# Performance work log

Measured on AMD Instinct MI355X. Metric: run time of the kernel, lower is better.

## Reference

```python
import jax, jax.numpy as jnp
import numpy as np

# Hardware-emulation constants (from init_kwargs, NeuroSim-style QLinear)
WL_IN = 8        # input activation bit width (bit-serial)
WL_W = 8         # weight bit width
CELL_BIT = 2     # bits per memory cell -> 4 weight slices
SUB = 128        # crossbar sub-array size (rows summed in analog)
ADC_BITS = 5     # ADC precision per partial sum
ONOFF = 10.0     # cell on/off conductance ratio
VARI = 0.05      # multiplicative device variation sigma


def _adc_quant(x, bits, axes):
    # LinearQuantizeOut: uniform quantization between tensor min/max
    mn = jnp.min(x, axis=axes, keepdims=True)
    mx = jnp.max(x, axis=axes, keepdims=True)
    step = (mx - mn) * (2.0 ** (-bits))
    step = jnp.where(step <= 0, 1.0, step)
    idx = jnp.clip(jnp.floor((x - mn) / step), 0.0, 2.0 ** bits - 1.0)
    return idx * step + mn


def _qlinear_hw(x, w, noise):
    """Analog PIM crossbar emulation of y = x @ w.T with bit-serial inputs,
    bit-sliced cells, on/off-ratio offset + dummy column, device variation,
    per-subarray ADC quantization."""
    B, N = x.shape
    F = w.shape[0]
    I, W, K = WL_IN, WL_W, WL_W // CELL_BIT
    cr = 2.0 ** CELL_BIT
    lower, upper = 1.0 / ONOFF, 1.0
    S = (N + SUB - 1) // SUB
    Np = S * SUB
    # quantize input to I bits in [0,1]; weight to W-bit integer in [0, 2^W-1]
    xq = jnp.round(jnp.clip(x, 0.0, 1.0) * (2.0 ** I - 1.0))            # [B, N]
    Xi = jnp.clip(jnp.round((w + 1.0) * 0.5 * (2.0 ** W - 1.0)), 0.0, 2.0 ** W - 1.0)  # [F, N]
    xq = jnp.pad(xq, ((0, 0), (0, Np - N)))
    Xi = jnp.pad(Xi, ((0, 0), (0, Np - N)))
    zpow = 2.0 ** jnp.arange(I, dtype=x.dtype)
    kpow = cr ** jnp.arange(K, dtype=x.dtype)
    bits = jnp.mod(jnp.floor(xq[..., None] / zpow), 2.0)                # [B, Np, I]
    slc = jnp.mod(jnp.floor(Xi[..., None] / kpow), cr)                  # [F, Np, K]
    g = slc * (upper - lower) + (cr - 1.0) * lower                      # cell conductances
    g = g * (1.0 + VARI * noise)                                        # device variation
    bits = bits.reshape(B, S, SUB, I)
    g = g.reshape(F, S, SUB, K)
    # analog partial sums per (input bit i, subarray s, weight slice k)
    P = jnp.einsum('bsai,fsak->iskbf', bits, g)                         # [I,S,K,B,F]
    # dummy column (all cells at lowest conductance), identical across F
    D = jnp.transpose(bits.sum(axis=2), (2, 1, 0)) * ((cr - 1.0) * lower)  # [I,S,B]
    Pq = _adc_quant(P, ADC_BITS, axes=(3, 4))
    Dq = _adc_quant(D, ADC_BITS, axes=(2,))
    scal = (2.0 ** jnp.arange(I, dtype=x.dtype))[:, None] * (cr ** jnp.arange(K, dtype=x.dtype))[None, :]
    acc = jnp.einsum('iskbf,ik->bf', Pq - Dq[:, :, None, :, None], scal) / (upper - lower)
    # undo integer mappings: w = 2*Xi/(2^W-1) - 1, x = xq/(2^I-1)
    out = 2.0 * acc / ((2.0 ** I - 1.0) * (2.0 ** W - 1.0)) \
          - xq.sum(axis=1, keepdims=True) / (2.0 ** I - 1.0)
    return out


def _qlinear(x, w, noise):
    # straight-through quantized weight (WAGE-style STE) + hardware forward
    Xi = jnp.clip(jnp.round((w + 1.0) * 0.5 * (2.0 ** WL_W - 1.0)), 0.0, 2.0 ** WL_W - 1.0)
    wq = 2.0 * Xi / (2.0 ** WL_W - 1.0) - 1.0
    wq_ste = w + jax.lax.stop_gradient(wq - w)
    out_ideal = x @ wq_ste.T
    out_hw = _qlinear_hw(x, w, noise)
    return out_ideal + jax.lax.stop_gradient(out_hw - out_ideal)


def setup_inputs() -> dict:
    key = jax.random.key(0)
    k1, k2, k3, k4, k5 = jax.random.split(key, 5)
    x = jax.random.uniform(k1, (1024, 784), dtype=jnp.float32)
    w1 = jax.random.normal(k2, (512, 784), dtype=jnp.float32) * 0.05
    w3 = jax.random.normal(k3, (10, 512), dtype=jnp.float32) * 0.08
    noise1 = jax.random.normal(k4, (512, 896, 4), dtype=jnp.float32)  # 784 padded to 7*128
    noise3 = jax.random.normal(k5, (10, 512, 4), dtype=jnp.float32)   # 512 = 4*128 exact
    return {"x": x, "w1": w1, "w3": w3, "noise1": noise1, "noise3": noise3}


def reference(x, w1, w3, noise1, noise3):
    h = jnp.tanh(_qlinear(x, w1, noise1))   # QLinear(784,512) + Tanh
    return _qlinear(h, w3, noise3)          # QLinear(512,10)
```

## Files before the change

kernel.cpp:

```cpp
#include <hip/hip_runtime.h>

#define FLTMAX 3.402823466e+38f


__global__ void init_kernel(float* __restrict__ acc1, unsigned* __restrict__ stats1)
{
    int gid = blockIdx.x * 256 + threadIdx.x;
    if (gid < 1024 * 512) acc1[gid] = 0.f;
    if (gid < 224) { stats1[gid * 2] = 0x7F7FFFFFu; stats1[gid * 2 + 1] = 0u; }
}

__global__ void prep1_kernel(const float* __restrict__ x, float* __restrict__ xq1,
                             float* __restrict__ sx1)
{
    __shared__ float red[128];
    int b = blockIdx.x;
    float psum = 0.f;
    for (int n = threadIdx.x; n < 896; n += 128) {
        float v = 0.f;
        if (n < 784) {
            float xv = x[b * 784 + n];
            xv = fminf(fmaxf(xv, 0.f), 1.f);
            v = rintf(__fmul_rn(xv, 255.f));
        }
        xq1[b * 896 + n] = v;
        psum += v;
    }
    red[threadIdx.x] = psum;
    __syncthreads();
    for (int w = 64; w >= 1; w >>= 1) {
        if (threadIdx.x < w) red[threadIdx.x] += red[threadIdx.x + w];
        __syncthreads();
    }
    if (threadIdx.x == 0) sx1[b] = red[0];
}

__global__ void bitpack_kernel(const float* __restrict__ xq1, unsigned* __restrict__ xqb)
{
    int gid = blockIdx.x * 256 + threadIdx.x;
    if (gid >= 1024 * 28) return;
    int b = gid / 28, w = gid % 28;
    unsigned words[8] = {0, 0, 0, 0, 0, 0, 0, 0};
    const float* src = &xq1[b * 896 + w * 32];
#pragma unroll 8
    for (int n = 0; n < 32; ++n) {
        int v = (int)src[n];
#pragma unroll
        for (int i = 0; i < 8; ++i) words[i] |= ((unsigned)((v >> i) & 1)) << n;
    }
#pragma unroll
    for (int i = 0; i < 8; ++i) xqb[(i * 1024 + b) * 28 + w] = words[i];
}

__global__ void prepg1t_kernel(const float* __restrict__ w1, const float* __restrict__ noise1,
                               float* __restrict__ g1t)
{
    __shared__ float t[4][32][33];
    const int n0 = blockIdx.x * 32, f0 = blockIdx.y * 32;
    const int tid = threadIdx.x;
    {
        int n = tid & 31, fi = tid >> 5;
#pragma unroll
        for (int p = 0; p < 4; ++p) {
            int f = p * 8 + fi;
            int gn = n0 + n, gf = f0 + f;
            float gv[4] = {0.f, 0.f, 0.f, 0.f};
            if (gn < 784) {
                float w = w1[gf * 784 + gn];
                float Xi = fminf(fmaxf(rintf(__fmul_rn(__fmul_rn(__fadd_rn(w, 1.f), 0.5f), 255.f)),
                                       0.f), 255.f);
                int xi = (int)Xi;
                float4 nz = *(const float4*)&noise1[(gf * 896 + gn) * 4];
                float nzv[4] = {nz.x, nz.y, nz.z, nz.w};
#pragma unroll
                for (int k = 0; k < 4; ++k) {
                    int slc = (xi >> (2 * k)) & 3;
                    float base = __fadd_rn(__fmul_rn((float)slc, 0.9f), 0.3f);
                    float nf = __fadd_rn(1.f, __fmul_rn(0.05f, nzv[k]));
                    gv[k] = __fmul_rn(base, nf);
                }
            }
#pragma unroll
            for (int k = 0; k < 4; ++k) t[k][n][f] = gv[k];
        }
    }
    __syncthreads();
    {
        int f = tid & 31, nn = tid >> 5;
#pragma unroll
        for (int p = 0; p < 4; ++p) {
            int n = p * 8 + nn;
#pragma unroll
            for (int k = 0; k < 4; ++k)
                g1t[(n0 + n) * 2048 + k * 512 + f0 + f] = t[k][n][f];
        }
    }
}

__global__ void prepg2_kernel(const float* __restrict__ w3, const float* __restrict__ noise3,
                              float* __restrict__ g2t)
{
    int gid = blockIdx.x * 256 + threadIdx.x;
    if (gid >= 10 * 512) return;
    int f = gid / 512, n = gid % 512;
    float w = w3[f * 512 + n];
    float Xi = fminf(fmaxf(rintf(__fmul_rn(__fmul_rn(__fadd_rn(w, 1.f), 0.5f), 255.f)),
                           0.f), 255.f);
    int xi = (int)Xi;
#pragma unroll
    for (int k = 0; k < 4; ++k) {
        int slc = (xi >> (2 * k)) & 3;
        float base = __fadd_rn(__fmul_rn((float)slc, 0.9f), 0.3f);
        float nf = __fadd_rn(1.f, __fmul_rn(0.05f, noise3[(f * 512 + n) * 4 + k]));
        g2t[n * 40 + k * 10 + f] = __fmul_rn(base, nf);
    }
}

__global__ void dq_kernel(const float* __restrict__ xq, float* __restrict__ Dq,
                          int S, int rowstride)
{
    __shared__ float red[512];
    const int i = blockIdx.x / S, s = blockIdx.x % S;
    const int tid = threadIdx.x;
    float D[4];
    float mn = FLTMAX, mx = -FLTMAX;
#pragma unroll
    for (int u = 0; u < 4; ++u) {
        int b = tid + u * 256;
        const float4* row = (const float4*)&xq[b * rowstride + s * 128];
        int c = 0;
#pragma unroll 8
        for (int q = 0; q < 32; ++q) {
            float4 v = row[q];
            c += (((int)v.x >> i) & 1) + (((int)v.y >> i) & 1) +
                 (((int)v.z >> i) & 1) + (((int)v.w >> i) & 1);
        }
        D[u] = __fmul_rn((float)c, 0.3f);
        mn = fminf(mn, D[u]);
        mx = fmaxf(mx, D[u]);
    }
    red[tid] = mn; red[256 + tid] = mx;
    __syncthreads();
    for (int w = 128; w >= 1; w >>= 1) {
        if (tid < w) {
            red[tid] = fminf(red[tid], red[tid + w]);
            red[256 + tid] = fmaxf(red[256 + tid], red[256 + tid + w]);
        }
        __syncthreads();
    }
    mn = red[0]; mx = red[256];
    float step = __fmul_rn(__fsub_rn(mx, mn), 0.03125f);
    if (step <= 0.f) step = 1.f;
#pragma unroll
    for (int u = 0; u < 4; ++u) {
        int b = tid + u * 256;
        float idx = fminf(fmaxf(floorf(__fdiv_rn(__fsub_rn(D[u], mn), step)), 0.f), 31.f);
        Dq[(i * S + s) * 1024 + b] = __fadd_rn(__fmul_rn(idx, step), mn);
    }
}

__global__ void dterm_kernel(const float* __restrict__ Dq, float* __restrict__ dterm, int S)
{
    int b = blockIdx.x * 256 + threadIdx.x;
    if (b >= 1024) return;
    float sum = 0.f;
    for (int i = 0; i < 8; ++i) {
        float sc = (float)(85 << i);
        for (int s = 0; s < S; ++s) sum = fmaf(Dq[(i * S + s) * 1024 + b], sc, sum);
    }
    dterm[b] = sum;
}

#define BK 32
__global__ __launch_bounds__(256, 4) void mm1_kernel(
    const unsigned* __restrict__ xqb, const float* __restrict__ g1t,
    float* __restrict__ P, unsigned* __restrict__ stats, int s, int i0)
{
    __shared__ __align__(16) float Bs[BK][132];
    __shared__ unsigned Abits[128];
    __shared__ float red[512];
    const int tid = threadIdx.x;
    const int il = blockIdx.x >> 3;
    const int i = i0 + il;
    const int b0 = (blockIdx.x & 7) * 128;
    const int colBase = blockIdx.y * 128;
    const int tx = tid & 15, ty = tid >> 4;

    const int aB = tid >> 5;
    const int eB = (tid & 31) << 2;

    float4 pB[4];
    unsigned pAw = 0;
#pragma unroll
    for (int u = 0; u < 4; ++u)
        pB[u] = *(const float4*)&g1t[(s * 128 + u * 8 + aB) * 2048 + colBase + eB];
    if (tid < 128) pAw = xqb[(i * 1024 + b0 + tid) * 28 + s * 4];

    float acc[8][8] = {};

    for (int ac = 0; ac < 4; ++ac) {
        __syncthreads();
#pragma unroll
        for (int u = 0; u < 4; ++u)
            *(float4*)&Bs[u * 8 + aB][eB] = pB[u];
        if (tid < 128) Abits[tid] = pAw;
        __syncthreads();

        if (ac < 3) {
            const int n0 = s * 128 + (ac + 1) * BK;
#pragma unroll
            for (int u = 0; u < 4; ++u)
                pB[u] = *(const float4*)&g1t[(n0 + u * 8 + aB) * 2048 + colBase + eB];
            if (tid < 128) pAw = xqb[(i * 1024 + b0 + tid) * 28 + s * 4 + ac + 1];
        }

        unsigned wrd[8];
#pragma unroll
        for (int u = 0; u < 4; ++u) {
            wrd[u]     = Abits[(ty << 2) + u];
            wrd[4 + u] = Abits[64 + (ty << 2) + u];
        }

#pragma unroll 4
        for (int a = 0; a < BK; ++a) {
            float br[8];
            *(float4*)&br[0] = *(const float4*)&Bs[a][(tx << 2)];
            *(float4*)&br[4] = *(const float4*)&Bs[a][64 + (tx << 2)];
#pragma unroll
            for (int u = 0; u < 8; ++u) {
                float ab = (float)((wrd[u] >> a) & 1u);
#pragma unroll
                for (int v = 0; v < 8; ++v)
                    acc[u][v] = fmaf(ab, br[v], acc[u][v]);
            }
        }
    }

#pragma unroll
    for (int uh = 0; uh < 2; ++uh)
#pragma unroll
        for (int u = 0; u < 4; ++u) {
            int row = il * 1024 + b0 + uh * 64 + (ty << 2) + u;
#pragma unroll
            for (int vh = 0; vh < 2; ++vh) {
                float4 v = make_float4(acc[uh * 4 + u][vh * 4 + 0], acc[uh * 4 + u][vh * 4 + 1],
                                       acc[uh * 4 + u][vh * 4 + 2], acc[uh * 4 + u][vh * 4 + 3]);
                *(float4*)&P[(size_t)row * 2048 + colBase + vh * 64 + (tx << 2)] = v;
            }
        }

    float mn = acc[0][0], mx = acc[0][0];
#pragma unroll
    for (int u = 0; u < 8; ++u)
#pragma unroll
        for (int v = 0; v < 8; ++v) { mn = fminf(mn, acc[u][v]); mx = fmaxf(mx, acc[u][v]); }
    red[tid] = mn; red[256 + tid] = mx;
    __syncthreads();
    for (int w = 128; w >= 1; w >>= 1) {
        if (tid < w) {
            red[tid] = fminf(red[tid], red[tid + w]);
            red[256 + tid] = fmaxf(red[256 + tid], red[256 + tid + w]);
        }
        __syncthreads();
    }
    if (tid == 0) {
        int k = colBase >> 9;
        int slot = ((s * 8 + i) * 4 + k) * 2;
        atomicMin(&stats[slot], __float_as_uint(red[0]));
        atomicMax(&stats[slot + 1], __float_as_uint(red[256]));
    }
}

__global__ void quant1_kernel(const float* __restrict__ P, const unsigned* __restrict__ stats,
                              float* __restrict__ acc1, int s, int i0, int ni)
{
    int gid = blockIdx.x * 256 + threadIdx.x;
    int b = gid >> 7, f4 = gid & 127;
    float4 sum = make_float4(0.f, 0.f, 0.f, 0.f);
    for (int il = 0; il < ni; ++il) {
        int i = i0 + il;
#pragma unroll
        for (int k = 0; k < 4; ++k) {
            int slot = ((s * 8 + i) * 4 + k) * 2;
            float mn = __uint_as_float(stats[slot]);
            float mx = __uint_as_float(stats[slot + 1]);
            float step = __fmul_rn(__fsub_rn(mx, mn), 0.03125f);
            if (step <= 0.f) step = 1.f;
            float4 val = *(const float4*)&P[(size_t)(il * 1024 + b) * 2048 + (k << 9) + (f4 << 2)];
            float sc = (float)(1 << (i + 2 * k));
            float ix, pq;
            ix = fminf(fmaxf(floorf(__fdiv_rn(__fsub_rn(val.x, mn), step)), 0.f), 31.f);
            pq = __fadd_rn(__fmul_rn(ix, step), mn); sum.x = fmaf(pq, sc, sum.x);
            ix = fminf(fmaxf(floorf(__fdiv_rn(__fsub_rn(val.y, mn), step)), 0.f), 31.f);
            pq = __fadd_rn(__fmul_rn(ix, step), mn); sum.y = fmaf(pq, sc, sum.y);
            ix = fminf(fmaxf(floorf(__fdiv_rn(__fsub_rn(val.z, mn), step)), 0.f), 31.f);
            pq = __fadd_rn(__fmul_rn(ix, step), mn); sum.z = fmaf(pq, sc, sum.z);
            ix = fminf(fmaxf(floorf(__fdiv_rn(__fsub_rn(val.w, mn), step)), 0.f), 31.f);
            pq = __fadd_rn(__fmul_rn(ix, step), mn); sum.w = fmaf(pq, sc, sum.w);
        }
    }
    float4* ap = (float4*)&acc1[(b << 9) + (f4 << 2)];
    float4 a = *ap;
    a.x += sum.x; a.y += sum.y; a.z += sum.z; a.w += sum.w;
    *ap = a;
}

__global__ void finish1_kernel(const float* __restrict__ acc1, const float* __restrict__ dterm1,
                               const float* __restrict__ sx1, float* __restrict__ xq2)
{
    int gid = blockIdx.x * 256 + threadIdx.x;
    int b = gid >> 9;
    float total = __fsub_rn(acc1[gid], dterm1[b]);
    float acc = __fdiv_rn(total, 0.9f);
    float o = __fsub_rn(__fdiv_rn(__fmul_rn(2.f, acc), 65025.f), __fdiv_rn(sx1[b], 255.f));
    float h = tanhf(o);
    h = fminf(fmaxf(h, 0.f), 1.f);
    xq2[gid] = rintf(__fmul_rn(h, 255.f));
}

__global__ void sx2_kernel(const float* __restrict__ xq2, float* __restrict__ sx2)
{
    __shared__ float red[128];
    int b = blockIdx.x;
    float psum = 0.f;
    for (int n = threadIdx.x; n < 512; n += 128) psum += xq2[b * 512 + n];
    red[threadIdx.x] = psum;
    __syncthreads();
    for (int w = 64; w >= 1; w >>= 1) {
        if (threadIdx.x < w) red[threadIdx.x] += red[threadIdx.x + w];
        __syncthreads();
    }
    if (threadIdx.x == 0) sx2[b] = red[0];
}

__global__ void mm2_kernel(const float* __restrict__ xq2, const float* __restrict__ g2t,
                           float* __restrict__ P2)
{
    int gid = blockIdx.x * 256 + threadIdx.x;
    if (gid >= 40960) return;
    int f = gid % 10;
    int b = (gid / 10) & 1023;
    int s = gid / 10240;
    float acc[8][4] = {};
    for (int a = 0; a < 128; ++a) {
        int n = s * 128 + a;
        int xi = (int)xq2[b * 512 + n];
        float g0 = g2t[n * 40 + f];
        float gA = g2t[n * 40 + 10 + f];
        float gB = g2t[n * 40 + 20 + f];
        float gC = g2t[n * 40 + 30 + f];
#pragma unroll
        for (int i = 0; i < 8; ++i) {
            float bi = (float)((xi >> i) & 1);
            acc[i][0] = fmaf(bi, g0, acc[i][0]);
            acc[i][1] = fmaf(bi, gA, acc[i][1]);
            acc[i][2] = fmaf(bi, gB, acc[i][2]);
            acc[i][3] = fmaf(bi, gC, acc[i][3]);
        }
    }
#pragma unroll
    for (int i = 0; i < 8; ++i)
#pragma unroll
        for (int k = 0; k < 4; ++k)
            P2[(size_t)((s * 8 + i) * 4 + k) * 10240 + b * 10 + f] = acc[i][k];
}

__global__ void stat2_kernel(const float* __restrict__ P2, float2* __restrict__ stats2)
{
    __shared__ float red[512];
    int p = blockIdx.x;
    int tid = threadIdx.x;
    float mn = FLTMAX, mx = -FLTMAX;
    for (int t = tid; t < 10240; t += 256) {
        float v = P2[(size_t)p * 10240 + t];
        mn = fminf(mn, v); mx = fmaxf(mx, v);
    }
    red[tid] = mn; red[256 + tid] = mx;
    __syncthreads();
    for (int w = 128; w >= 1; w >>= 1) {
        if (tid < w) {
            red[tid] = fminf(red[tid], red[tid + w]);
            red[256 + tid] = fmaxf(red[256 + tid], red[256 + tid + w]);
        }
        __syncthreads();
    }
    if (tid == 0) {
        float step = __fmul_rn(__fsub_rn(red[256], red[0]), 0.03125f);
        if (step <= 0.f) step = 1.f;
        stats2[p] = make_float2(red[0], step);
    }
}

__global__ void out2_kernel(const float* __restrict__ P2, const float2* __restrict__ stats2,
                            const float* __restrict__ dterm2, const float* __restrict__ sx2,
                            float* __restrict__ out)
{
    int gid = blockIdx.x * 256 + threadIdx.x;
    if (gid >= 10240) return;
    int b = gid / 10;
    float sum = 0.f;
    for (int s = 0; s < 4; ++s)
        for (int i = 0; i < 8; ++i)
#pragma unroll
            for (int k = 0; k < 4; ++k) {
                int p = (s * 8 + i) * 4 + k;
                float2 st = stats2[p];
                float val = P2[(size_t)p * 10240 + gid];
                float idx = fminf(fmaxf(floorf(__fdiv_rn(__fsub_rn(val, st.x), st.y)), 0.f), 31.f);
                float pq = __fadd_rn(__fmul_rn(idx, st.y), st.x);
                sum = fmaf(pq, (float)(1 << (i + 2 * k)), sum);
            }
    float total = __fsub_rn(sum, dterm2[b]);
    float acc = __fdiv_rn(total, 0.9f);
    out[gid] = __fsub_rn(__fdiv_rn(__fmul_rn(2.f, acc), 65025.f), __fdiv_rn(sx2[b], 255.f));
}

extern "C" void kernel_launch(void* const* d_in, const int* in_sizes, int n_in,
                              void* d_out, int out_size, void* d_ws, size_t ws_size,
                              hipStream_t stream)
{
    const float* x      = (const float*)d_in[0];
    const float* w1     = (const float*)d_in[1];
    const float* w3     = (const float*)d_in[2];
    const float* noise1 = (const float*)d_in[3];
    const float* noise3 = (const float*)d_in[4];
    float* out = (float*)d_out;
    float* ws  = (float*)d_ws;

    float*    xq1    = ws + 0;
    float*    g1t    = ws + 917504;
    float*    acc1   = ws + 2752512;
    float*    xq2    = ws + 3276800;
    float*    P2     = ws + 3801088;
    float*    g2t    = ws + 5111808;
    float*    Dq1    = ws + 5132288;
    float*    Dq2    = ws + 5189632;
    float*    sx1    = ws + 5222400;
    float*    sx2    = ws + 5223424;
    float*    dterm1 = ws + 5224448;
    float*    dterm2 = ws + 5225472;
    float2*   stats2 = (float2*)(ws + 5226496);
    unsigned* stats1 = (unsigned*)(ws + 5226752);
    unsigned* xqb    = (unsigned*)(ws + 5227264);
    float*    Ps     = ws + 5456640;

    const size_t fixedf = 5456640;
    int ni = 8;
    while (ni > 1 && (fixedf + (size_t)ni * 2097152) * sizeof(float) > ws_size) ni >>= 1;

    init_kernel<<<2048, 256, 0, stream>>>(acc1, stats1);
    prep1_kernel<<<1024, 128, 0, stream>>>(x, xq1, sx1);
    prepg1t_kernel<<<dim3(28, 16), 256, 0, stream>>>(w1, noise1, g1t);
    bitpack_kernel<<<112, 256, 0, stream>>>(xq1, xqb);
    dq_kernel<<<56, 256, 0, stream>>>(xq1, Dq1, 7, 896);
    dterm_kernel<<<4, 256, 0, stream>>>(Dq1, dterm1, 7);

    for (int s = 0; s < 7; ++s)
        for (int i0 = 0; i0 < 8; i0 += ni) {
            mm1_kernel<<<dim3(8 * ni, 16), 256, 0, stream>>>(xqb, g1t, Ps, stats1, s, i0);
            quant1_kernel<<<512, 256, 0, stream>>>(Ps, stats1, acc1, s, i0, ni);
        }

    finish1_kernel<<<2048, 256, 0, stream>>>(acc1, dterm1, sx1, xq2);
    sx2_kernel<<<1024, 128, 0, stream>>>(xq2, sx2);
    prepg2_kernel<<<20, 256, 0, stream>>>(w3, noise3, g2t);
    dq_kernel<<<32, 256, 0, stream>>>(xq2, Dq2, 4, 512);
    dterm_kernel<<<4, 256, 0, stream>>>(Dq2, dterm2, 4);
    mm2_kernel<<<160, 256, 0, stream>>>(xq2, g2t, P2);
    stat2_kernel<<<128, 256, 0, stream>>>(P2, stats2);
    out2_kernel<<<40, 256, 0, stream>>>(P2, stats2, dterm2, sx2, out);
}
```

Before: 757.8 us.

## Batch mm1/quant1 across subarrays, popcount bitplanes for dq, drop init kernel

Each mm1/quant1 launch now covers up to G subarrays with all eight bit planes, instead of one launch pair per subarray and bit group. This cuts the number of launches from 14 or more down to about 2 and lets quant1 write acc1 directly, so the zero-init kernel is gone. The stats1 init moves into prep1. The dq kernels now popcount the packed bitplanes instead of scanning float rows, and finish1 builds the layer-2 bitplanes with wave ballots. The cost is a much larger P workspace: G depends on ws_size and falls back to smaller groups if space is short.

```diff
diff --git a/kernel.cpp b/kernel.cpp
--- a/kernel.cpp
+++ b/kernel.cpp
@@ -3,18 +3,16 @@
 #define FLTMAX 3.402823466e+38f
 
 
-__global__ void init_kernel(float* __restrict__ acc1, unsigned* __restrict__ stats1)
-{
-    int gid = blockIdx.x * 256 + threadIdx.x;
-    if (gid < 1024 * 512) acc1[gid] = 0.f;
-    if (gid < 224) { stats1[gid * 2] = 0x7F7FFFFFu; stats1[gid * 2 + 1] = 0u; }
-}
-
 __global__ void prep1_kernel(const float* __restrict__ x, float* __restrict__ xq1,
-                             float* __restrict__ sx1)
+                             float* __restrict__ sx1, unsigned* __restrict__ stats1)
 {
     __shared__ float red[128];
     int b = blockIdx.x;
+    if (blockIdx.x == 0) {
+        for (int t = threadIdx.x; t < 224; t += 128) {
+            stats1[t * 2] = 0x7F7FFFFFu; stats1[t * 2 + 1] = 0u;
+        }
+    }
     float psum = 0.f;
     for (int n = threadIdx.x; n < 896; n += 128) {
         float v = 0.f;
@@ -116,8 +114,8 @@
     }
 }
 
-__global__ void dq_kernel(const float* __restrict__ xq, float* __restrict__ Dq,
-                          int S, int rowstride)
+__global__ void dqpop_kernel(const unsigned* __restrict__ xqb, float* __restrict__ Dq,
+                             int S, int wpr)
 {
     __shared__ float red[512];
     const int i = blockIdx.x / S, s = blockIdx.x % S;
@@ -127,14 +125,8 @@
 #pragma unroll
     for (int u = 0; u < 4; ++u) {
         int b = tid + u * 256;
-        const float4* row = (const float4*)&xq[b * rowstride + s * 128];
-        int c = 0;
-#pragma unroll 8
-        for (int q = 0; q < 32; ++q) {
-            float4 v = row[q];
-            c += (((int)v.x >> i) & 1) + (((int)v.y >> i) & 1) +
-                 (((int)v.z >> i) & 1) + (((int)v.w >> i) & 1);
-        }
+        uint4 w = *(const uint4*)&xqb[(i * 1024 + b) * wpr + s * 4];
+        int c = __popc(w.x) + __popc(w.y) + __popc(w.z) + __popc(w.w);
         D[u] = __fmul_rn((float)c, 0.3f);
         mn = fminf(mn, D[u]);
         mx = fmaxf(mx, D[u]);
@@ -174,15 +166,17 @@
 #define BK 32
 __global__ __launch_bounds__(256, 4) void mm1_kernel(
     const unsigned* __restrict__ xqb, const float* __restrict__ g1t,
-    float* __restrict__ P, unsigned* __restrict__ stats, int s, int i0)
+    float* __restrict__ P, unsigned* __restrict__ stats, int s0)
 {
     __shared__ __align__(16) float Bs[BK][132];
     __shared__ unsigned Abits[128];
     __shared__ float red[512];
     const int tid = threadIdx.x;
-    const int il = blockIdx.x >> 3;
-    const int i = i0 + il;
-    const int b0 = (blockIdx.x & 7) * 128;
+    const int sl = blockIdx.x >> 6;
+    const int r = blockIdx.x & 63;
+    const int i = r >> 3;
+    const int b0 = (r & 7) * 128;
+    const int s = s0 + sl;
     const int colBase = blockIdx.y * 128;
     const int tx = tid & 15, ty = tid >> 4;
 
@@ -240,7 +234,7 @@
     for (int uh = 0; uh < 2; ++uh)
 #pragma unroll
         for (int u = 0; u < 4; ++u) {
-            int row = il * 1024 + b0 + uh * 64 + (ty << 2) + u;
+            int row = (sl * 8 + i) * 1024 + b0 + uh * 64 + (ty << 2) + u;
 #pragma unroll
             for (int vh = 0; vh < 2; ++vh) {
                 float4 v = make_float4(acc[uh * 4 + u][vh * 4 + 0], acc[uh * 4 + u][vh * 4 + 1],
@@ -272,50 +266,69 @@
 }
 
 __global__ void quant1_kernel(const float* __restrict__ P, const unsigned* __restrict__ stats,
-                              float* __restrict__ acc1, int s, int i0, int ni)
+                              float* __restrict__ acc1, int s0, int G, int first)
 {
     int gid = blockIdx.x * 256 + threadIdx.x;
     int b = gid >> 7, f4 = gid & 127;
-    float4 sum = make_float4(0.f, 0.f, 0.f, 0.f);
-    for (int il = 0; il < ni; ++il) {
-        int i = i0 + il;
-#pragma unroll
-        for (int k = 0; k < 4; ++k) {
-            int slot = ((s * 8 + i) * 4 + k) * 2;
-            float mn = __uint_as_float(stats[slot]);
-            float mx = __uint_as_float(stats[slot + 1]);
-            float step = __fmul_rn(__fsub_rn(mx, mn), 0.03125f);
-            if (step <= 0.f) step = 1.f;
-            float4 val = *(const float4*)&P[(size_t)(il * 1024 + b) * 2048 + (k << 9) + (f4 << 2)];
-            float sc = (float)(1 << (i + 2 * k));
-            float ix, pq;
-            ix = fminf(fmaxf(floorf(__fdiv_rn(__fsub_rn(val.x, mn), step)), 0.f), 31.f);
-            pq = __fadd_rn(__fmul_rn(ix, step), mn); sum.x = fmaf(pq, sc, sum.x);
-            ix = fminf(fmaxf(floorf(__fdiv_rn(__fsub_rn(val.y, mn), step)), 0.f), 31.f);
-            pq = __fadd_rn(__fmul_rn(ix, step), mn); sum.y = fmaf(pq, sc, sum.y);
-            ix = fminf(fmaxf(floorf(__fdiv_rn(__fsub_rn(val.z, mn), step)), 0.f), 31.f);
-            pq = __fadd_rn(__fmul_rn(ix, step), mn); sum.z = fmaf(pq, sc, sum.z);
-            ix = fminf(fmaxf(floorf(__fdiv_rn(__fsub_rn(val.w, mn), step)), 0.f), 31.f);
-            pq = __fadd_rn(__fmul_rn(ix, step), mn); sum.w = fmaf(pq, sc, sum.w);
-        }
-    }
-    float4* ap = (float4*)&acc1[(b << 9) + (f4 << 2)];
-    float4 a = *ap;
-    a.x += sum.x; a.y += sum.y; a.z += sum.z; a.w += sum.w;
-    *ap = a;
+    float4 accR;
+    if (first) accR = make_float4(0.f, 0.f, 0.f, 0.f);
+    else       accR = *(const float4*)&acc1[(b << 9) + (f4 << 2)];
+    for (int sl = 0; sl < G; ++sl) {
+        int s = s0 + sl;
+        float4 sum = make_float4(0.f, 0.f, 0.f, 0.f);
+        for (int i = 0; i < 8; ++i) {
+#pragma unroll
+            for (int k = 0; k < 4; ++k) {
+                int slot = ((s * 8 + i) * 4 + k) * 2;
+                float mn = __uint_as_float(stats[slot]);
+                float mx = __uint_as_float(stats[slot + 1]);
+                float step = __fmul_rn(__fsub_rn(mx, mn), 0.03125f);
+                if (step <= 0.f) step = 1.f;
+                float4 val = *(const float4*)&P[(size_t)((sl * 8 + i) * 1024 + b) * 2048
+                                                + (k << 9) + (f4 << 2)];
+                float sc = (float)(1 << (i + 2 * k));
+                float ix, pq;
+                ix = fminf(fmaxf(floorf(__fdiv_rn(__fsub_rn(val.x, mn), step)), 0.f), 31.f);
+                pq = __fadd_rn(__fmul_rn(ix, step), mn); sum.x = fmaf(pq, sc, sum.x);
+                ix = fminf(fmaxf(floorf(__fdiv_rn(__fsub_rn(val.y, mn), step)), 0.f), 31.f);
+                pq = __fadd_rn(__fmul_rn(ix, step), mn); sum.y = fmaf(pq, sc, sum.y);
+                ix = fminf(fmaxf(floorf(__fdiv_rn(__fsub_rn(val.z, mn), step)), 0.f), 31.f);
+                pq = __fadd_rn(__fmul_rn(ix, step), mn); sum.z = fmaf(pq, sc, sum.z);
+                ix = fminf(fmaxf(floorf(__fdiv_rn(__fsub_rn(val.w, mn), step)), 0.f), 31.f);
+                pq = __fadd_rn(__fmul_rn(ix, step), mn); sum.w = fmaf(pq, sc, sum.w);
+            }
+        }
+        accR.x = __fadd_rn(accR.x, sum.x);
+        accR.y = __fadd_rn(accR.y, sum.y);
+        accR.z = __fadd_rn(accR.z, sum.z);
+        accR.w = __fadd_rn(accR.w, sum.w);
+    }
+    *(float4*)&acc1[(b << 9) + (f4 << 2)] = accR;
 }
 
 __global__ void finish1_kernel(const float* __restrict__ acc1, const float* __restrict__ dterm1,
-                               const float* __restrict__ sx1, float* __restrict__ xq2)
-{
-    int gid = blockIdx.x * 256 + threadIdx.x;
-    int b = gid >> 9;
+                               const float* __restrict__ sx1, float* __restrict__ xq2,
+                               unsigned* __restrict__ xqb2)
+{
+    int gid = blockIdx.x * 256 + threadIdx.x;
+    int b = gid >> 9, f = gid & 511;
     float total = __fsub_rn(acc1[gid], dterm1[b]);
     float acc = __fdiv_rn(total, 0.9f);
     float o = __fsub_rn(__fdiv_rn(__fmul_rn(2.f, acc), 65025.f), __fdiv_rn(sx1[b], 255.f));
     float h = tanhf(o);
     h = fminf(fmaxf(h, 0.f), 1.f);
-    xq2[gid] = rintf(__fmul_rn(h, 255.f));
+    float code = rintf(__fmul_rn(h, 255.f));
+    xq2[gid] = code;
+    int ci = (int)code;
+    int lane = threadIdx.x & 63;
+#pragma unroll
+    for (int i = 0; i < 8; ++i) {
+        unsigned long long m = __ballot((ci >> i) & 1);
+        if ((lane & 31) == 0) {
+            unsigned wv = (lane & 32) ? (unsigned)(m >> 32) : (unsigned)m;
+            xqb2[(i * 1024 + b) * 16 + (f >> 5)] = wv;
+        }
+    }
 }
 
 __global__ void sx2_kernel(const float* __restrict__ xq2, float* __restrict__ sx2)
@@ -442,29 +455,30 @@
     float2*   stats2 = (float2*)(ws + 5226496);
     unsigned* stats1 = (unsigned*)(ws + 5226752);
     unsigned* xqb    = (unsigned*)(ws + 5227264);
-    float*    Ps     = ws + 5456640;
-
-    const size_t fixedf = 5456640;
-    int ni = 8;
-    while (ni > 1 && (fixedf + (size_t)ni * 2097152) * sizeof(float) > ws_size) ni >>= 1;
-
-    init_kernel<<<2048, 256, 0, stream>>>(acc1, stats1);
-    prep1_kernel<<<1024, 128, 0, stream>>>(x, xq1, sx1);
+    unsigned* xqb2   = (unsigned*)(ws + 5456640);
+    float*    Ps     = ws + 5587712;
+
+    const size_t fixedf = 5587712;
+    const size_t planef = 16777216;
+    int G = 1;
+    while (G < 7 && (fixedf + (size_t)(G + 1) * planef) * sizeof(float) <= ws_size) ++G;
+
+    prep1_kernel<<<1024, 128, 0, stream>>>(x, xq1, sx1, stats1);
     prepg1t_kernel<<<dim3(28, 16), 256, 0, stream>>>(w1, noise1, g1t);
     bitpack_kernel<<<112, 256, 0, stream>>>(xq1, xqb);
-    dq_kernel<<<56, 256, 0, stream>>>(xq1, Dq1, 7, 896);
+    dqpop_kernel<<<56, 256, 0, stream>>>(xqb, Dq1, 7, 28);
     dterm_kernel<<<4, 256, 0, stream>>>(Dq1, dterm1, 7);
 
-    for (int s = 0; s < 7; ++s)
-        for (int i0 = 0; i0 < 8; i0 += ni) {
-            mm1_kernel<<<dim3(8 * ni, 16), 256, 0, stream>>>(xqb, g1t, Ps, stats1, s, i0);
-            quant1_kernel<<<512, 256, 0, stream>>>(Ps, stats1, acc1, s, i0, ni);
-        }
-
-    finish1_kernel<<<2048, 256, 0, stream>>>(acc1, dterm1, sx1, xq2);
+    for (int s0 = 0; s0 < 7; s0 += G) {
+        int Gc = (7 - s0 < G) ? (7 - s0) : G;
+        mm1_kernel<<<dim3(Gc * 64, 16), 256, 0, stream>>>(xqb, g1t, Ps, stats1, s0);
+        quant1_kernel<<<512, 256, 0, stream>>>(Ps, stats1, acc1, s0, Gc, s0 == 0);
+    }
+
+    finish1_kernel<<<2048, 256, 0, stream>>>(acc1, dterm1, sx1, xq2, xqb2);
     sx2_kernel<<<1024, 128, 0, stream>>>(xq2, sx2);
     prepg2_kernel<<<20, 256, 0, stream>>>(w3, noise3, g2t);
-    dq_kernel<<<32, 256, 0, stream>>>(xq2, Dq2, 4, 512);
+    dqpop_kernel<<<32, 256, 0, stream>>>(xqb2, Dq2, 4, 16);
     dterm_kernel<<<4, 256, 0, stream>>>(Dq2, dterm2, 4);
     mm2_kernel<<<160, 256, 0, stream>>>(xq2, g2t, P2);
     stat2_kernel<<<128, 256, 0, stream>>>(P2, stats2);
```

New measurement: 668.1 us. 11.8% less time.
